# Optimization experiments

Hardware: AMD Instinct MI355X
Metric: run time of the kernel (lower is better)

The kernel has to match this reference:

```python
import jax, jax.numpy as jnp
import numpy as np

N = 50000
E = 800000
IN_DIM = 256
OUT_DIM = 64
ALPHA = 0.2  # LeakyReLU negative slope
EPS = 9e-15


def setup_inputs() -> dict:
    key = jax.random.key(0)
    k1, k2, k3, k4 = jax.random.split(key, 4)
    x = jax.random.normal(k1, (N, IN_DIM), dtype=jnp.float32)
    edge = jax.random.randint(k2, (2, E), 0, N, dtype=jnp.int32)
    # xavier_normal with gain=1.414
    gain = 1.414
    W = jax.random.normal(k3, (IN_DIM, OUT_DIM), dtype=jnp.float32) * (gain * np.sqrt(2.0 / (IN_DIM + OUT_DIM)))
    attn = jax.random.normal(k4, (1, 2 * OUT_DIM), dtype=jnp.float32) * (gain * np.sqrt(2.0 / (1 + 2 * OUT_DIM)))
    return {"x": x, "edge": edge, "W": W, "attn": attn}


def reference(x, edge, W, attn):
    n = x.shape[0]
    h = x @ W                                   # [N, D]
    src, dst = edge[0], edge[1]
    d = h.shape[1]
    a_src = attn[0, :d]                         # attn . concat(h_src, h_dst) split
    a_dst = attn[0, d:]
    s = h @ a_src                               # [N]
    t = h @ a_dst                               # [N]
    values = s[src] + t[dst]                    # [E] per-edge attention logits
    edge_e_a = jnp.where(values >= 0, values, ALPHA * values)  # LeakyReLU
    edge_e = jnp.exp(edge_e_a - jnp.max(edge_e_a))              # [E]
    # scatter-sum over destination rows (edge[0] is the output row in spmm)
    e_rowsum = jax.ops.segment_sum(edge_e, src, num_segments=n)[:, None]  # [N,1]
    msgs = edge_e[:, None] * h[dst]             # [E, D] gathered messages
    h_prime = jax.ops.segment_sum(msgs, src, num_segments=n)              # [N, D]
    h_prime = h_prime / (e_rowsum + EPS)
    return h_prime
```

## Files before the change

### kernel.cpp

```cpp
#include <hip/hip_runtime.h>
#include <stdint.h>

#define NN 50000
#define NE 800000
#define KDIM 256
#define DDIM 64
#define ALPHA 0.2f
#define EPSV 9e-15f

#define NBIN 512
#define BSPAN 98
#define SPAN2 49
#define BCAP 2048
#define HCAP 1024
#define PBLK 256
#define EPB 3125
#define GEMM_BLOCKS 1024
#define FGRID (PBLK + GEMM_BLOCKS)

#define O_S    0
#define O_T    50000
#define O_HB   100000
#define O_WB   1700000
#define O_BIN  1708192
#define O_EBUF 1708704

typedef __bf16 bf16x8 __attribute__((ext_vector_type(8)));
typedef float f32x4 __attribute__((ext_vector_type(4)));

__device__ __forceinline__ ushort f2bf(float f) {
    uint32_t u = __float_as_uint(f);
    return (ushort)((u + 0x7fffu + ((u >> 16) & 1u)) >> 16);
}
__device__ __forceinline__ float bf2f(ushort u) {
    return __uint_as_float(((uint32_t)u) << 16);
}
__device__ __forceinline__ uint binof(uint src) {
    return (src * 85599u) >> 23;
}

__global__ __launch_bounds__(256) void k_prep(const float* __restrict__ W,
                                              uint* __restrict__ BINCNT,
                                              uint4* __restrict__ WB) {
    const int g = blockIdx.x * 256 + threadIdx.x;
    if (g < NBIN) BINCNT[g] = 0u;
    if (g < 2048) {
        int ts = g >> 6;
        int ln = g & 63;
        int s = ts >> 2, t = ts & 3;
        int q = ln >> 4, c = ln & 15;
        union { ushort us[8]; uint4 v; } pk;
#pragma unroll
        for (int j = 0; j < 8; ++j) {
            int k = s * 32 + q * 8 + j;
            pk.us[j] = f2bf(W[k * DDIM + t * 16 + c]);
        }
        WB[g] = pk.v;
    }
}

__global__ __launch_bounds__(256) void k_fused(const float* __restrict__ X,
                                               const uint4* __restrict__ WB,
                                               const float* __restrict__ attn,
                                               const int* __restrict__ edge,
                                               ushort* __restrict__ HB,
                                               float* __restrict__ S,
                                               float* __restrict__ T,
                                               uint* __restrict__ BINCNT,
                                               uint* __restrict__ EBUF) {
    __shared__ uint4 bsm[2048];

    if (blockIdx.x < PBLK) {
        uint* sm = (uint*)bsm;
        const int CNT0 = 0, BST = 512, GBS = 1024, STG = 1536, SRT = 4672;
        const int tid = threadIdx.x;
        for (int b = tid; b < NBIN; b += 256) sm[CNT0 + b] = 0u;
        __syncthreads();
        const int p0 = blockIdx.x * EPB;
        for (int k = tid; k < EPB; k += 256) {
            uint s = (uint)edge[p0 + k];
            uint d = (uint)edge[NE + p0 + k];
            sm[STG + k] = s | (d << 16);
            atomicAdd(&sm[CNT0 + binof(s)], 1u);
        }
        __syncthreads();
        if (tid < 64) {
            uint carry = 0;
            for (int c = 0; c < 8; ++c) {
                uint v = sm[CNT0 + c * 64 + tid];
                uint incl = v;
#pragma unroll
                for (int m = 1; m < 64; m <<= 1) {
                    uint t = __shfl_up(incl, m, 64);
                    if (tid >= m) incl += t;
                }
                sm[BST + c * 64 + tid] = incl - v + carry;
                carry += __shfl(incl, 63, 64);
            }
        }
        __syncthreads();
        for (int b = tid; b < NBIN; b += 256) {
            uint c = sm[CNT0 + b];
            sm[GBS + b] = c ? atomicAdd(&BINCNT[b], c) : 0u;
            sm[CNT0 + b] = sm[BST + b];
        }
        __syncthreads();
        for (int k = tid; k < EPB; k += 256) {
            uint pk = sm[STG + k];
            uint bin = binof(pk & 0xffffu);
            uint slot = atomicAdd(&sm[CNT0 + bin], 1u);
            sm[SRT + slot] = pk;
        }
        __syncthreads();
        for (int k = tid; k < EPB; k += 256) {
            int lo = 0, hi = NBIN - 1;
            while (lo < hi) {
                int mid = (lo + hi + 1) >> 1;
                if (sm[BST + mid] <= (uint)k) lo = mid; else hi = mid - 1;
            }
            uint local = (uint)k - sm[BST + lo] + sm[GBS + lo];
            if (local < BCAP) EBUF[lo * BCAP + local] = sm[SRT + k];
        }
        return;
    }

    uint4 wreg[8];
#pragma unroll
    for (int j = 0; j < 8; ++j) wreg[j] = WB[j * 256 + threadIdx.x];
#pragma unroll
    for (int j = 0; j < 8; ++j) bsm[j * 256 + threadIdx.x] = wreg[j];
    __syncthreads();

    const int lane = threadIdx.x & 63;
    const int wave = (blockIdx.x - PBLK) * 4 + (threadIdx.x >> 6);
    const int nwaves = GEMM_BLOCKS * 4;
    const int quad = lane >> 4;
    const int nn = lane & 15;

    float asrc[4], adst[4];
#pragma unroll
    for (int t = 0; t < 4; ++t) {
        asrc[t] = attn[t * 16 + nn];
        adst[t] = attn[DDIM + t * 16 + nn];
    }

    const int MT = NN / 16;
    for (int mt = wave; mt < MT; mt += nwaves) {
        const int row0 = mt * 16;
        const float* xr = X + (size_t)(row0 + nn) * KDIM + quad * 8;
        bf16x8 afrag[8];
#pragma unroll
        for (int s = 0; s < 8; ++s) {
            float4 lo = *reinterpret_cast<const float4*>(xr + s * 32);
            float4 hi = *reinterpret_cast<const float4*>(xr + s * 32 + 4);
            union { ushort u[8]; bf16x8 v; } aa;
            aa.u[0] = f2bf(lo.x); aa.u[1] = f2bf(lo.y);
            aa.u[2] = f2bf(lo.z); aa.u[3] = f2bf(lo.w);
            aa.u[4] = f2bf(hi.x); aa.u[5] = f2bf(hi.y);
            aa.u[6] = f2bf(hi.z); aa.u[7] = f2bf(hi.w);
            afrag[s] = aa.v;
        }

        f32x4 acc[4];
#pragma unroll
        for (int t = 0; t < 4; ++t) acc[t] = {0.f, 0.f, 0.f, 0.f};
#pragma unroll
        for (int s = 0; s < 8; ++s)
#pragma unroll
            for (int t = 0; t < 4; ++t) {
                bf16x8 bf = *reinterpret_cast<const bf16x8*>(
                    &bsm[(s * 4 + t) * 64 + lane]);
                acc[t] = __builtin_amdgcn_mfma_f32_16x16x32_bf16(
                    afrag[s], bf, acc[t], 0, 0, 0);
            }

#pragma unroll
        for (int t = 0; t < 4; ++t)
#pragma unroll
            for (int r = 0; r < 4; ++r)
                HB[(size_t)(row0 + quad * 4 + r) * DDIM + t * 16 + nn] =
                    f2bf(acc[t][r]);

        float sp[4], tp[4];
#pragma unroll
        for (int r = 0; r < 4; ++r) { sp[r] = 0.f; tp[r] = 0.f; }
#pragma unroll
        for (int t = 0; t < 4; ++t)
#pragma unroll
            for (int r = 0; r < 4; ++r) {
                sp[r] = fmaf(acc[t][r], asrc[t], sp[r]);
                tp[r] = fmaf(acc[t][r], adst[t], tp[r]);
            }
#pragma unroll
        for (int m = 1; m < 16; m <<= 1)
#pragma unroll
            for (int r = 0; r < 4; ++r) {
                sp[r] += __shfl_xor(sp[r], m, 64);
                tp[r] += __shfl_xor(tp[r], m, 64);
            }
        if (nn == 0) {
#pragma unroll
            for (int r = 0; r < 4; ++r) {
                S[row0 + quad * 4 + r] = sp[r];
                T[row0 + quad * 4 + r] = tp[r];
            }
        }
    }
}

__global__ __launch_bounds__(512) void k_agg(const uint* __restrict__ EBUF,
                                             const uint* __restrict__ BINCNT,
                                             const float* __restrict__ S,
                                             const float* __restrict__ T,
                                             const ushort* __restrict__ HB,
                                             float* __restrict__ out) {
    __shared__ uint2 sDE[HCAP];
    __shared__ uint  cntL[SPAN2];
    __shared__ uint  off[SPAN2 + 1];
    __shared__ uint  cur[SPAN2];
    __shared__ float Sseg[SPAN2];

    const int b = blockIdx.x >> 1;
    const int half = blockIdx.x & 1;
    const int nb0 = b * BSPAN + half * SPAN2;
    const int tid = threadIdx.x;

    if (tid < SPAN2) {
        cntL[tid] = 0u;
        int node = nb0 + tid;
        Sseg[tid] = (node < NN) ? S[node] : 0.f;
    }
    __syncthreads();

    int cnt = (int)BINCNT[b];
    cnt = cnt < BCAP ? cnt : BCAP;
    const uint* eb = EBUF + b * BCAP;

    for (int k = tid; k < cnt; k += 512) {
        int row = (int)(eb[k] & 0xffffu) - nb0;
        if ((unsigned)row < SPAN2) atomicAdd(&cntL[row], 1u);
    }
    __syncthreads();

    if (tid < 64) {
        uint v = (tid < SPAN2) ? cntL[tid] : 0u;
        uint incl = v;
#pragma unroll
        for (int m = 1; m < 64; m <<= 1) {
            uint t = __shfl_up(incl, m, 64);
            if (tid >= m) incl += t;
        }
        if (tid < SPAN2) { off[tid] = incl - v; cur[tid] = incl - v; }
        if (tid == SPAN2 - 1) off[SPAN2] = incl;
    }
    __syncthreads();

    for (int k = tid; k < cnt; k += 512) {
        uint pk = eb[k];
        int row = (int)(pk & 0xffffu) - nb0;
        if ((unsigned)row < SPAN2) {
            float v = Sseg[row] + T[pk >> 16];
            float a = v >= 0.f ? v : ALPHA * v;
            float e = __expf(a);
            uint pos = atomicAdd(&cur[row], 1u);
            sDE[pos] = make_uint2(pk >> 16, __float_as_uint(e));
        }
    }
    __syncthreads();

    const int wv = tid >> 6;
    const int lane = tid & 63;
    const int sub = lane >> 5;
    const int c2 = lane & 31;
    const ushort* hb2 = HB + 2 * c2;

    for (int r = wv; r < SPAN2; r += 8) {
        const int start = (int)off[r];
        const int deg = (int)(off[r + 1] - off[r]);
        float a0 = 0.f, a1 = 0.f, rs = 0.f;
        for (int j = 0; j < deg; j += 16) {
            uint dd[8]; float ee[8];
#pragma unroll
            for (int u = 0; u < 8; ++u) {
                int idx = j + 2 * u + sub;
                int ic = start + (idx < deg ? idx : 0);
                uint2 q = sDE[ic];
                dd[u] = q.x;
                ee[u] = (idx < deg) ? __uint_as_float(q.y) : 0.f;
            }
            __builtin_amdgcn_sched_barrier(0);
            float f0[8], f1[8];
#pragma unroll
            for (int u = 0; u < 8; ++u) {
                uint g2 = *reinterpret_cast<const uint*>(
                    hb2 + (size_t)dd[u] * DDIM);
                f0[u] = bf2f((ushort)(g2 & 0xffffu));
                f1[u] = bf2f((ushort)(g2 >> 16));
            }
            __builtin_amdgcn_sched_barrier(0);
#pragma unroll
            for (int u = 0; u < 8; ++u) {
                a0 = fmaf(ee[u], f0[u], a0);
                a1 = fmaf(ee[u], f1[u], a1);
                rs += ee[u];
            }
        }
        a0 += __shfl_xor(a0, 32, 64);
        a1 += __shfl_xor(a1, 32, 64);
        rs += __shfl_xor(rs, 32, 64);
        const int node = nb0 + r;
        if (sub == 0 && node < NN) {
            float inv = 1.f / (rs + EPSV);
            reinterpret_cast<float2*>(out + (size_t)node * DDIM)[c2] =
                make_float2(a0 * inv, a1 * inv);
        }
    }
}

extern "C" void kernel_launch(void* const* d_in, const int* in_sizes, int n_in,
                              void* d_out, int out_size, void* d_ws, size_t ws_size,
                              hipStream_t stream) {
    const float* X    = (const float*)d_in[0];
    const int*   edge = (const int*)d_in[1];
    const float* W    = (const float*)d_in[2];
    const float* attn = (const float*)d_in[3];

    uint*   wu = (uint*)d_ws;
    float*  wf = (float*)d_ws;
    float*  S      = wf + O_S;
    float*  T      = wf + O_T;
    ushort* HB     = (ushort*)(wu + O_HB);
    uint4*  WB     = (uint4*)(wu + O_WB);
    uint*   BINCNT = wu + O_BIN;
    uint*   EBUF   = wu + O_EBUF;

    k_prep<<<8, 256, 0, stream>>>(W, BINCNT, WB);
    k_fused<<<FGRID, 256, 0, stream>>>(X, WB, attn, edge, HB, S, T, BINCNT, EBUF);
    k_agg<<<NBIN * 2, 512, 0, stream>>>(EBUF, BINCNT, S, T, HB, (float*)d_out);
}
```

Baseline: 131.4 us.

## Rebalance partition/GEMM blocks, drop binary search in scatter, use packed bf16 convert

```diff
diff --git a/kernel.cpp b/kernel.cpp
--- a/kernel.cpp
+++ b/kernel.cpp
@@ -13,9 +13,9 @@
 #define SPAN2 49
 #define BCAP 2048
 #define HCAP 1024
-#define PBLK 256
-#define EPB 3125
-#define GEMM_BLOCKS 1024
+#define PBLK 512
+#define EPB 1563
+#define GEMM_BLOCKS 784
 #define FGRID (PBLK + GEMM_BLOCKS)
 
 #define O_S    0
@@ -72,12 +72,13 @@
 
     if (blockIdx.x < PBLK) {
         uint* sm = (uint*)bsm;
-        const int CNT0 = 0, BST = 512, GBS = 1024, STG = 1536, SRT = 4672;
+        const int CNT0 = 0, BST = 512, GBS = 1024, STG = 1536, SRT = 3099;
         const int tid = threadIdx.x;
+        const int p0 = blockIdx.x * EPB;
+        const int nv = (NE - p0) < EPB ? (NE - p0) : EPB;
         for (int b = tid; b < NBIN; b += 256) sm[CNT0 + b] = 0u;
         __syncthreads();
-        const int p0 = blockIdx.x * EPB;
-        for (int k = tid; k < EPB; k += 256) {
+        for (int k = tid; k < nv; k += 256) {
             uint s = (uint)edge[p0 + k];
             uint d = (uint)edge[NE + p0 + k];
             sm[STG + k] = s | (d << 16);
@@ -105,21 +106,18 @@
             sm[CNT0 + b] = sm[BST + b];
         }
         __syncthreads();
-        for (int k = tid; k < EPB; k += 256) {
+        for (int k = tid; k < nv; k += 256) {
             uint pk = sm[STG + k];
             uint bin = binof(pk & 0xffffu);
             uint slot = atomicAdd(&sm[CNT0 + bin], 1u);
             sm[SRT + slot] = pk;
         }
         __syncthreads();
-        for (int k = tid; k < EPB; k += 256) {
-            int lo = 0, hi = NBIN - 1;
-            while (lo < hi) {
-                int mid = (lo + hi + 1) >> 1;
-                if (sm[BST + mid] <= (uint)k) lo = mid; else hi = mid - 1;
-            }
-            uint local = (uint)k - sm[BST + lo] + sm[GBS + lo];
-            if (local < BCAP) EBUF[lo * BCAP + local] = sm[SRT + k];
+        for (int k = tid; k < nv; k += 256) {
+            uint pk = sm[SRT + k];
+            uint bin = binof(pk & 0xffffu);
+            uint local = (uint)k - sm[BST + bin] + sm[GBS + bin];
+            if (local < BCAP) EBUF[bin * BCAP + local] = pk;
         }
         return;
     }
@@ -153,11 +151,15 @@
         for (int s = 0; s < 8; ++s) {
             float4 lo = *reinterpret_cast<const float4*>(xr + s * 32);
             float4 hi = *reinterpret_cast<const float4*>(xr + s * 32 + 4);
-            union { ushort u[8]; bf16x8 v; } aa;
-            aa.u[0] = f2bf(lo.x); aa.u[1] = f2bf(lo.y);
-            aa.u[2] = f2bf(lo.z); aa.u[3] = f2bf(lo.w);
-            aa.u[4] = f2bf(hi.x); aa.u[5] = f2bf(hi.y);
-            aa.u[6] = f2bf(hi.z); aa.u[7] = f2bf(hi.w);
+            union { uint u[4]; bf16x8 v; } aa;
+            asm("v_cvt_pk_bf16_f32 %0, %1, %2"
+                : "=v"(aa.u[0]) : "v"(lo.x), "v"(lo.y));
+            asm("v_cvt_pk_bf16_f32 %0, %1, %2"
+                : "=v"(aa.u[1]) : "v"(lo.z), "v"(lo.w));
+            asm("v_cvt_pk_bf16_f32 %0, %1, %2"
+                : "=v"(aa.u[2]) : "v"(hi.x), "v"(hi.y));
+            asm("v_cvt_pk_bf16_f32 %0, %1, %2"
+                : "=v"(aa.u[3]) : "v"(hi.z), "v"(hi.w));
             afrag[s] = aa.v;
         }
 
```

New measurement: 139.0 us. 1.06x slower.
